# Optimization experiments

Measured on AMD Instinct MI355X. Metric: run time of the kernel, lower is better.

The kernel has to match this reference:

```python
import jax, jax.numpy as jnp
import numpy as np

B, F, N = 64, 32, 36
REGION, HIDDEN, ATT = 1024, 1024, 1024
FEAT2 = REGION + 2 * HIDDEN  # temp_attn feat_size = 3072


def setup_inputs() -> dict:
    key = jax.random.key(0)
    ks = jax.random.split(key, 12)
    s = 0.02
    return {
        "frame_feats": jax.random.normal(ks[0], (B, F, 2 * HIDDEN), jnp.float32),
        "object_feats": jax.random.normal(ks[1], (B, F, N, REGION), jnp.float32),
        "hidden_state": jax.random.normal(ks[2], (B, HIDDEN), jnp.float32),
        # spatial attention params (torch Linear: y = x @ W.T + b)
        "s_wh_w": jax.random.normal(ks[3], (ATT, HIDDEN), jnp.float32) * s,
        "s_wh_b": jnp.zeros((ATT,), jnp.float32),
        "s_wv_w": jax.random.normal(ks[4], (ATT, REGION), jnp.float32) * s,
        "s_wv_b": jnp.zeros((ATT,), jnp.float32),
        "s_wa_w": jax.random.normal(ks[5], (ATT,), jnp.float32) * s,
        # temporal attention params (att_size = hidden_size here)
        "t_wh_w": jax.random.normal(ks[6], (HIDDEN, HIDDEN), jnp.float32) * s,
        "t_wh_b": jnp.zeros((HIDDEN,), jnp.float32),
        "t_wv_w": jax.random.normal(ks[7], (HIDDEN, FEAT2), jnp.float32) * s,
        "t_wv_b": jnp.zeros((HIDDEN,), jnp.float32),
        "t_wa_w": jax.random.normal(ks[8], (HIDDEN,), jnp.float32) * s,
    }


def reference(frame_feats, object_feats, hidden_state,
              s_wh_w, s_wh_b, s_wv_w, s_wv_b, s_wa_w,
              t_wh_w, t_wh_b, t_wv_w, t_wv_b, t_wa_w):
    # ---- spatial attention over num_boxes, per (batch, frame) ----
    # v: [B,F,N,ATT]; key proj broadcasts over frames and boxes
    v = jnp.einsum('bfnd,ad->bfna', object_feats, s_wv_w) + s_wv_b
    h = hidden_state @ s_wh_w.T + s_wh_b            # [B,ATT]
    score = jnp.tanh(v + h[:, None, None, :]) @ s_wa_w  # [B,F,N]
    alpha = jax.nn.softmax(score, axis=-1)
    obj_att = jnp.einsum('bfn,bfnd->bfd', alpha, object_feats)  # [B,F,REGION]

    # ---- temporal attention over frames ----
    feat = jnp.concatenate([obj_att, frame_feats], axis=-1)     # [B,F,FEAT2]
    v2 = jnp.einsum('bfd,ad->bfa', feat, t_wv_w) + t_wv_b       # [B,F,HIDDEN]
    h2 = hidden_state @ t_wh_w.T + t_wh_b                       # [B,HIDDEN]
    score2 = jnp.tanh(v2 + h2[:, None, :]) @ t_wa_w             # [B,F]
    beta = jax.nn.softmax(score2, axis=-1)
    loc_feat = jnp.einsum('bf,bfd->bd', beta, feat)             # [B,FEAT2]
    return loc_feat
```

## Files before the change

### kernel.cpp

```cpp
#include <hip/hip_runtime.h>
#include <hip/hip_bf16.h>
#include <stdint.h>

#define BATCH  64
#define NFRAME 32
#define NBOX   36
#define REGION 1024
#define HIDDEN 1024
#define ATTSZ  1024
#define FEAT2  3072
#define M_S (BATCH * NFRAME * NBOX)
#define M_T (BATCH * NFRAME)

typedef __attribute__((ext_vector_type(8))) short bf16x8;
typedef __attribute__((ext_vector_type(4))) float f32x4;

__device__ __forceinline__ unsigned short f2bf(float f) {
  union { float f; uint32_t u; } v; v.f = f;
  return (unsigned short)((v.u + 0x7FFFu + ((v.u >> 16) & 1u)) >> 16);
}
__device__ __forceinline__ float bf2f(unsigned short u) {
  union { uint32_t u; float f; } v; v.u = (uint32_t)u << 16; return v.f;
}
__device__ __forceinline__ float fast_tanh(float x) {
  float e = __expf(2.f * x);
  return 1.f - 2.f / (e + 1.f);
}
__device__ __forceinline__ void gload_lds16(const unsigned short* g, unsigned short* l) {
  __builtin_amdgcn_global_load_lds(
      (const __attribute__((address_space(1))) unsigned int*)g,
      (__attribute__((address_space(3))) unsigned int*)l, 16, 0, 0);
}

__global__ __launch_bounds__(256) void cast_f32_bf16(
    const float* __restrict__ in, unsigned short* __restrict__ out, long n) {
  long i = ((long)blockIdx.x * 256 + threadIdx.x) * 8;
  if (i >= n) return;
  float4 a = *(const float4*)(in + i);
  float4 b = *(const float4*)(in + i + 4);
  ushort4 lo; lo.x = f2bf(a.x); lo.y = f2bf(a.y); lo.z = f2bf(a.z); lo.w = f2bf(a.w);
  ushort4 hi; hi.x = f2bf(b.x); hi.y = f2bf(b.y); hi.z = f2bf(b.z); hi.w = f2bf(b.w);
  *(ushort4*)(out + i) = lo;
  *(ushort4*)(out + i + 4) = hi;
}

template<int TM, int TN>
__global__ __launch_bounds__(256, 2) void gemm_tanh_score(
    const unsigned short* __restrict__ A, const unsigned short* __restrict__ W,
    const float* __restrict__ hvec, const float* __restrict__ wa,
    float* __restrict__ score, int K, int rows_per_b)
{
  constexpr int BM = 2 * TM * 16;
  constexpr int BN = 2 * TN * 16;
  __shared__ __align__(16) unsigned short ldsA[BM * 64];
  __shared__ __align__(16) unsigned short ldsW[BN * 64];
  __shared__ float h_tile[BN];
  __shared__ float score_sh[2][BM];

  const int tid  = threadIdx.x;
  const int lane = tid & 63;
  const int wid  = tid >> 6;
  const int wr   = (wid >> 1) * (TM * 16);
  const int wc   = (wid & 1) * (TN * 16);
  const int l15  = lane & 15;
  const int q    = lane >> 4;
  const long r0  = (long)blockIdx.y * BM;
  const int  c0  = blockIdx.x * BN;
  const int srow = lane >> 3;
  const int sgr  = lane & 7;
  const int b0   = (int)(r0 / rows_per_b);

  for (int i = tid; i < BN; i += 256)
    h_tile[i] = hvec[(long)b0 * ATTSZ + c0 + i];
  float wac[TN];
  #pragma unroll
  for (int j = 0; j < TN; ++j) wac[j] = wa[c0 + wc + j * 16 + l15];

  f32x4 acc[TM][TN] = {};

  for (int k0 = 0; k0 < K; k0 += 64) {
    __syncthreads();
    #pragma unroll
    for (int it = 0; it < BM / 32; ++it) {
      int c = wid * (BM / 32) + it;
      gload_lds16(A + (r0 + c * 8 + srow) * (long)K + k0 + sgr * 8, ldsA + c * 512);
    }
    #pragma unroll
    for (int it = 0; it < BN / 32; ++it) {
      int c = wid * (BN / 32) + it;
      gload_lds16(W + ((long)(c0 + c * 8 + srow)) * K + k0 + sgr * 8, ldsW + c * 512);
    }
    __syncthreads();
    #pragma unroll
    for (int s = 0; s < 2; ++s) {
      bf16x8 af[TM], wf[TN];
      #pragma unroll
      for (int i = 0; i < TM; ++i)
        af[i] = *(const bf16x8*)(ldsA + (wr + i * 16 + l15) * 64 + s * 32 + q * 8);
      #pragma unroll
      for (int j = 0; j < TN; ++j)
        wf[j] = *(const bf16x8*)(ldsW + (wc + j * 16 + l15) * 64 + s * 32 + q * 8);
      #pragma unroll
      for (int i = 0; i < TM; ++i)
        #pragma unroll
        for (int j = 0; j < TN; ++j)
          acc[i][j] = __builtin_amdgcn_mfma_f32_16x16x32_bf16(af[i], wf[j], acc[i][j], 0, 0, 0);
    }
  }

  #pragma unroll
  for (int i = 0; i < TM; ++i) {
    #pragma unroll
    for (int r = 0; r < 4; ++r) {
      float part = 0.f;
      #pragma unroll
      for (int j = 0; j < TN; ++j) {
        float x = acc[i][j][r] + h_tile[wc + j * 16 + l15];
        part += fast_tanh(x) * wac[j];
      }
      part += __shfl_xor(part, 1); part += __shfl_xor(part, 2);
      part += __shfl_xor(part, 4); part += __shfl_xor(part, 8);
      if (l15 == 0) score_sh[wid & 1][wr + i * 16 + q * 4 + r] = part;
    }
  }
  __syncthreads();
  if (tid < BM)
    atomicAdd(score + r0 + tid, score_sh[0][tid] + score_sh[1][tid]);
}

__global__ __launch_bounds__(256) void hidden_proj(
    const float* __restrict__ hidden,
    const float* __restrict__ s_wh_w, const float* __restrict__ s_wh_b,
    const float* __restrict__ s_wv_b,
    const float* __restrict__ t_wh_w, const float* __restrict__ t_wh_b,
    const float* __restrict__ t_wv_b,
    float* __restrict__ h_s, float* __restrict__ h_t)
{
  const float *W, *b1, *b2;
  float* out;
  if (blockIdx.y == 0) { W = s_wh_w; b1 = s_wh_b; b2 = s_wv_b; out = h_s; }
  else                 { W = t_wh_w; b1 = t_wh_b; b2 = t_wv_b; out = h_t; }
  const int lane = threadIdx.x & 63;
  const int wid  = threadIdx.x >> 6;
  const int a    = blockIdx.x * 4 + wid;
  __shared__ float hs[64 * 256];
  float acc[64];
  #pragma unroll
  for (int b = 0; b < 64; ++b) acc[b] = 0.f;

  for (int dc = 0; dc < 4; ++dc) {
    __syncthreads();
    for (int i = threadIdx.x; i < 4096; i += 256) {
      int b = i >> 6, d4 = i & 63;
      *(float4*)(hs + b * 256 + d4 * 4) =
          *(const float4*)(hidden + b * 1024 + dc * 256 + d4 * 4);
    }
    __syncthreads();
    float4 w4 = *(const float4*)(W + (long)a * 1024 + dc * 256 + lane * 4);
    #pragma unroll
    for (int b = 0; b < 64; ++b) {
      float4 h4 = *(const float4*)(hs + b * 256 + lane * 4);
      acc[b] += w4.x * h4.x + w4.y * h4.y + w4.z * h4.z + w4.w * h4.w;
    }
  }
  #pragma unroll
  for (int b = 0; b < 64; ++b) {
    #pragma unroll
    for (int off = 1; off < 64; off <<= 1)
      acc[b] += __shfl_xor(acc[b], off);
  }
  float res = 0.f;
  #pragma unroll
  for (int b = 0; b < 64; ++b)
    if (lane == b) res = acc[b];
  out[lane * 1024 + a] = res + b1[a] + b2[a];
}

__global__ __launch_bounds__(256) void spatial_softmax_obj_bf16(
    const unsigned short* __restrict__ objb, const float* __restrict__ score,
    const float* __restrict__ frame, float* __restrict__ feat,
    unsigned short* __restrict__ featb)
{
  const int bf = blockIdx.x;
  __shared__ float alpha[NBOX];
  if (threadIdx.x < 64) {
    int n = threadIdx.x;
    float v = (n < NBOX) ? score[bf * NBOX + n] : -1e30f;
    float m = v;
    #pragma unroll
    for (int off = 32; off; off >>= 1) m = fmaxf(m, __shfl_xor(m, off));
    float e = (n < NBOX) ? __expf(v - m) : 0.f;
    float ssum = e;
    #pragma unroll
    for (int off = 32; off; off >>= 1) ssum += __shfl_xor(ssum, off);
    if (n < NBOX) alpha[n] = e / ssum;
  }
  __syncthreads();
  const unsigned short* base = objb + (long)bf * NBOX * REGION;
  float4 av = {0.f, 0.f, 0.f, 0.f};
  for (int n = 0; n < NBOX; ++n) {
    float al = alpha[n];
    ushort4 o = *(const ushort4*)(base + n * REGION + threadIdx.x * 4);
    av.x += al * bf2f(o.x); av.y += al * bf2f(o.y);
    av.z += al * bf2f(o.z); av.w += al * bf2f(o.w);
  }
  float* frow = feat + (long)bf * FEAT2;
  unsigned short* fbrow = featb + (long)bf * FEAT2;
  *(float4*)(frow + threadIdx.x * 4) = av;
  ushort4 avb; avb.x = f2bf(av.x); avb.y = f2bf(av.y); avb.z = f2bf(av.z); avb.w = f2bf(av.w);
  *(ushort4*)(fbrow + threadIdx.x * 4) = avb;
  const float* fsrc = frame + (long)bf * 2 * HIDDEN;
  #pragma unroll
  for (int c = 0; c < 2; ++c) {
    float4 v = *(const float4*)(fsrc + (threadIdx.x + c * 256) * 4);
    *(float4*)(frow + REGION + (threadIdx.x + c * 256) * 4) = v;
    ushort4 vb; vb.x = f2bf(v.x); vb.y = f2bf(v.y); vb.z = f2bf(v.z); vb.w = f2bf(v.w);
    *(ushort4*)(fbrow + REGION + (threadIdx.x + c * 256) * 4) = vb;
  }
}

__global__ __launch_bounds__(256) void temporal_out(
    const float* __restrict__ score2, const float* __restrict__ feat,
    float* __restrict__ out)
{
  const int b = blockIdx.x;
  __shared__ float beta[NFRAME];
  if (threadIdx.x < 64) {
    int f = threadIdx.x;
    float v = (f < NFRAME) ? score2[b * NFRAME + f] : -1e30f;
    float m = v;
    #pragma unroll
    for (int off = 32; off; off >>= 1) m = fmaxf(m, __shfl_xor(m, off));
    float e = (f < NFRAME) ? __expf(v - m) : 0.f;
    float ssum = e;
    #pragma unroll
    for (int off = 32; off; off >>= 1) ssum += __shfl_xor(ssum, off);
    if (f < NFRAME) beta[f] = e / ssum;
  }
  __syncthreads();
  #pragma unroll
  for (int c = 0; c < 3; ++c) {
    int col = (threadIdx.x + c * 256) * 4;
    float4 av = {0.f, 0.f, 0.f, 0.f};
    for (int f = 0; f < NFRAME; ++f) {
      float bw = beta[f];
      float4 v = *(const float4*)(feat + (long)(b * NFRAME + f) * FEAT2 + col);
      av.x += bw * v.x; av.y += bw * v.y; av.z += bw * v.z; av.w += bw * v.w;
    }
    *(float4*)(out + (long)b * FEAT2 + col) = av;
  }
}

#define FBM 128
#define FBN 128
#define FBK 64
#define LDKP 72
__global__ __launch_bounds__(256) void fused_gemm_tanh_score_f32(
    const float* __restrict__ A, const float* __restrict__ W,
    const float* __restrict__ hvec, const float* __restrict__ wa,
    float* __restrict__ score, int M, int K, int rows_per_b)
{
  __shared__ unsigned short ldsA[FBM * LDKP];
  __shared__ unsigned short ldsW[FBN * LDKP];
  const int tid  = threadIdx.x;
  const int lane = tid & 63;
  const int wid  = tid >> 6;
  const int wr   = (wid >> 1) * 64;
  const int wc   = (wid & 1) * 64;
  const int l15  = lane & 15;
  const int q    = lane >> 4;
  const long r0  = (long)blockIdx.y * FBM;
  const int  c0  = blockIdx.x * FBN;

  f32x4 acc[4][4] = {};
  for (int k0 = 0; k0 < K; k0 += FBK) {
    __syncthreads();
    #pragma unroll
    for (int it = 0; it < 8; ++it) {
      int c = tid + it * 256;
      int row = c >> 4, qb = c & 15;
      float4 s = *(const float4*)(A + (r0 + row) * (long)K + k0 + qb * 4);
      ushort4 d; d.x = f2bf(s.x); d.y = f2bf(s.y); d.z = f2bf(s.z); d.w = f2bf(s.w);
      *(ushort4*)(ldsA + row * LDKP + qb * 4) = d;
    }
    #pragma unroll
    for (int it = 0; it < 8; ++it) {
      int c = tid + it * 256;
      int row = c >> 4, qb = c & 15;
      float4 s = *(const float4*)(W + (c0 + row) * (long)K + k0 + qb * 4);
      ushort4 d; d.x = f2bf(s.x); d.y = f2bf(s.y); d.z = f2bf(s.z); d.w = f2bf(s.w);
      *(ushort4*)(ldsW + row * LDKP + qb * 4) = d;
    }
    __syncthreads();
    #pragma unroll
    for (int s = 0; s < 2; ++s) {
      bf16x8 af[4], bfr[4];
      #pragma unroll
      for (int i = 0; i < 4; ++i)
        af[i] = *(const bf16x8*)(ldsA + (wr + i * 16 + l15) * LDKP + s * 32 + q * 8);
      #pragma unroll
      for (int j = 0; j < 4; ++j)
        bfr[j] = *(const bf16x8*)(ldsW + (wc + j * 16 + l15) * LDKP + s * 32 + q * 8);
      #pragma unroll
      for (int i = 0; i < 4; ++i)
        #pragma unroll
        for (int j = 0; j < 4; ++j)
          acc[i][j] = __builtin_amdgcn_mfma_f32_16x16x32_bf16(af[i], bfr[j], acc[i][j], 0, 0, 0);
    }
  }
  float wac[4];
  #pragma unroll
  for (int j = 0; j < 4; ++j) wac[j] = wa[c0 + wc + j * 16 + l15];
  #pragma unroll
  for (int i = 0; i < 4; ++i) {
    #pragma unroll
    for (int r = 0; r < 4; ++r) {
      int row = (int)r0 + wr + i * 16 + q * 4 + r;
      const float* hrow = hvec + (long)(row / rows_per_b) * ATTSZ;
      float part = 0.f;
      #pragma unroll
      for (int j = 0; j < 4; ++j) {
        float x = acc[i][j][r] + hrow[c0 + wc + j * 16 + l15];
        part += fast_tanh(x) * wac[j];
      }
      part += __shfl_xor(part, 1); part += __shfl_xor(part, 2);
      part += __shfl_xor(part, 4); part += __shfl_xor(part, 8);
      if (l15 == 0) atomicAdd(score + row, part);
    }
  }
}

__global__ __launch_bounds__(256) void spatial_softmax_obj_f32(
    const float* __restrict__ obj, const float* __restrict__ score,
    const float* __restrict__ frame, float* __restrict__ feat)
{
  const int bf = blockIdx.x;
  __shared__ float alpha[NBOX];
  if (threadIdx.x < 64) {
    int n = threadIdx.x;
    float v = (n < NBOX) ? score[bf * NBOX + n] : -1e30f;
    float m = v;
    #pragma unroll
    for (int off = 32; off; off >>= 1) m = fmaxf(m, __shfl_xor(m, off));
    float e = (n < NBOX) ? __expf(v - m) : 0.f;
    float ssum = e;
    #pragma unroll
    for (int off = 32; off; off >>= 1) ssum += __shfl_xor(ssum, off);
    if (n < NBOX) alpha[n] = e / ssum;
  }
  __syncthreads();
  const float* base = obj + (long)bf * NBOX * REGION;
  float4 av = {0.f, 0.f, 0.f, 0.f};
  for (int n = 0; n < NBOX; ++n) {
    float al = alpha[n];
    float4 o = *(const float4*)(base + n * REGION + threadIdx.x * 4);
    av.x += al * o.x; av.y += al * o.y; av.z += al * o.z; av.w += al * o.w;
  }
  float* frow = feat + (long)bf * FEAT2;
  *(float4*)(frow + threadIdx.x * 4) = av;
  const float4* fsrc = (const float4*)(frame + (long)bf * 2 * HIDDEN);
  float4* fdst = (float4*)(frow + REGION);
  fdst[threadIdx.x]       = fsrc[threadIdx.x];
  fdst[threadIdx.x + 256] = fsrc[threadIdx.x + 256];
}

extern "C" void kernel_launch(void* const* d_in, const int* in_sizes, int n_in,
                              void* d_out, int out_size, void* d_ws, size_t ws_size,
                              hipStream_t stream) {
  const float* frame  = (const float*)d_in[0];
  const float* obj    = (const float*)d_in[1];
  const float* hidden = (const float*)d_in[2];
  const float* s_wh_w = (const float*)d_in[3];
  const float* s_wh_b = (const float*)d_in[4];
  const float* s_wv_w = (const float*)d_in[5];
  const float* s_wv_b = (const float*)d_in[6];
  const float* s_wa_w = (const float*)d_in[7];
  const float* t_wh_w = (const float*)d_in[8];
  const float* t_wh_b = (const float*)d_in[9];
  const float* t_wv_w = (const float*)d_in[10];
  const float* t_wv_b = (const float*)d_in[11];
  const float* t_wa_w = (const float*)d_in[12];
  float* out = (float*)d_out;

  char* p = (char*)d_ws;
  auto alloc = [&](size_t bytes) { char* r = p; p += (bytes + 255) & ~255ull; return r; };
  float* h_s     = (float*)alloc(65536 * 4);
  float* h_t     = (float*)alloc(65536 * 4);
  float* score_s = (float*)alloc((size_t)M_S * 4);
  float* score2  = (float*)alloc((size_t)M_T * 4);
  float* feat    = (float*)alloc((size_t)M_T * FEAT2 * 4);
  unsigned short* objb  = (unsigned short*)alloc((size_t)M_S * REGION * 2);
  unsigned short* featb = (unsigned short*)alloc((size_t)M_T * FEAT2 * 2);
  unsigned short* wvsb  = (unsigned short*)alloc((size_t)ATTSZ * REGION * 2);
  unsigned short* wvtb  = (unsigned short*)alloc((size_t)HIDDEN * FEAT2 * 2);
  size_t needed = (size_t)(p - (char*)d_ws);
  bool fast = needed <= ws_size;

  hipMemsetAsync(score_s, 0, (size_t)(M_S + M_T) * sizeof(float), stream);
  hidden_proj<<<dim3(256, 2), 256, 0, stream>>>(
      hidden, s_wh_w, s_wh_b, s_wv_b, t_wh_w, t_wh_b, t_wv_b, h_s, h_t);

  if (fast) {
    cast_f32_bf16<<<(M_S * (long)REGION) / 2048, 256, 0, stream>>>(obj, objb, (long)M_S * REGION);
    cast_f32_bf16<<<(ATTSZ * (long)REGION) / 2048, 256, 0, stream>>>(s_wv_w, wvsb, (long)ATTSZ * REGION);
    cast_f32_bf16<<<(HIDDEN * (long)FEAT2) / 2048, 256, 0, stream>>>(t_wv_w, wvtb, (long)HIDDEN * FEAT2);

    gemm_tanh_score<4, 8><<<dim3(4, M_S / 128), 256, 0, stream>>>(
        objb, wvsb, h_s, s_wa_w, score_s, REGION, NFRAME * NBOX);

    spatial_softmax_obj_bf16<<<M_T, 256, 0, stream>>>(objb, score_s, frame, feat, featb);

    gemm_tanh_score<1, 4><<<dim3(8, M_T / 32), 256, 0, stream>>>(
        featb, wvtb, h_t, t_wa_w, score2, FEAT2, NFRAME);
  } else {
    fused_gemm_tanh_score_f32<<<dim3(8, M_S / FBM), 256, 0, stream>>>(
        obj, s_wv_w, h_s, s_wa_w, score_s, M_S, REGION, NFRAME * NBOX);
    spatial_softmax_obj_f32<<<M_T, 256, 0, stream>>>(obj, score_s, frame, feat);
    fused_gemm_tanh_score_f32<<<dim3(8, M_T / FBM), 256, 0, stream>>>(
        feat, t_wv_w, h_t, t_wa_w, score2, M_T, FEAT2, NFRAME);
  }

  temporal_out<<<BATCH, 256, 0, stream>>>(score2, feat, out);
}
```

Measured before the change: 789.5 us.

## Swizzle LDS tiles in bf16 GEMM and remap spatial grid for cache locality

Applies an XOR swizzle to the 16-byte chunk index of each row, both when global_load_lds writes the A and W tiles into LDS and when the MFMA fragments are read back. This is meant to remove LDS bank conflicts on the fragment reads. The spatial GEMM also moves to a 1D grid whose block index is remapped so that groups of 8 row tiles sweep all 4 column tiles together, improving L2 reuse of the object tiles. Small unroll pragmas are added to the softmax-weighted reduction loops.

```diff
diff --git a/kernel.cpp b/kernel.cpp
--- a/kernel.cpp
+++ b/kernel.cpp
@@ -44,7 +44,7 @@
   *(ushort4*)(out + i + 4) = hi;
 }
 
-template<int TM, int TN>
+template<int TM, int TN, bool LINGRID, int NCOLT>
 __global__ __launch_bounds__(256, 2) void gemm_tanh_score(
     const unsigned short* __restrict__ A, const unsigned short* __restrict__ W,
     const float* __restrict__ hvec, const float* __restrict__ wa,
@@ -64,11 +64,20 @@
   const int wc   = (wid & 1) * (TN * 16);
   const int l15  = lane & 15;
   const int q    = lane >> 4;
-  const long r0  = (long)blockIdx.y * BM;
-  const int  c0  = blockIdx.x * BN;
+  const int rl   = l15 & 7;
   const int srow = lane >> 3;
-  const int sgr  = lane & 7;
-  const int b0   = (int)(r0 / rows_per_b);
+  const int sgr  = (lane & 7) ^ srow;
+
+  long r0; int c0;
+  if (LINGRID) {
+    int bid = blockIdx.x;
+    int rt = (bid & 7) + (bid >> (3 + (NCOLT == 4 ? 2 : 3))) * 8;
+    int ct = (bid >> 3) & (NCOLT - 1);
+    r0 = (long)rt * BM; c0 = ct * BN;
+  } else {
+    r0 = (long)blockIdx.y * BM; c0 = blockIdx.x * BN;
+  }
+  const int b0 = (int)(r0 / rows_per_b);
 
   for (int i = tid; i < BN; i += 256)
     h_tile[i] = hvec[(long)b0 * ATTSZ + c0 + i];
@@ -83,23 +92,24 @@
     #pragma unroll
     for (int it = 0; it < BM / 32; ++it) {
       int c = wid * (BM / 32) + it;
-      gload_lds16(A + (r0 + c * 8 + srow) * (long)K + k0 + sgr * 8, ldsA + c * 512);
+      gload_lds16(A + (r0 + c * 8 + srow) * (long)K + k0 + (sgr << 3), ldsA + c * 512);
     }
     #pragma unroll
     for (int it = 0; it < BN / 32; ++it) {
       int c = wid * (BN / 32) + it;
-      gload_lds16(W + ((long)(c0 + c * 8 + srow)) * K + k0 + sgr * 8, ldsW + c * 512);
+      gload_lds16(W + ((long)(c0 + c * 8 + srow)) * K + k0 + (sgr << 3), ldsW + c * 512);
     }
     __syncthreads();
     #pragma unroll
     for (int s = 0; s < 2; ++s) {
       bf16x8 af[TM], wf[TN];
+      const int gsw = ((s * 4 + q) ^ rl) << 3;
       #pragma unroll
       for (int i = 0; i < TM; ++i)
-        af[i] = *(const bf16x8*)(ldsA + (wr + i * 16 + l15) * 64 + s * 32 + q * 8);
+        af[i] = *(const bf16x8*)(ldsA + (wr + i * 16 + l15) * 64 + gsw);
       #pragma unroll
       for (int j = 0; j < TN; ++j)
-        wf[j] = *(const bf16x8*)(ldsW + (wc + j * 16 + l15) * 64 + s * 32 + q * 8);
+        wf[j] = *(const bf16x8*)(ldsW + (wc + j * 16 + l15) * 64 + gsw);
       #pragma unroll
       for (int i = 0; i < TM; ++i)
         #pragma unroll
@@ -198,6 +208,7 @@
   __syncthreads();
   const unsigned short* base = objb + (long)bf * NBOX * REGION;
   float4 av = {0.f, 0.f, 0.f, 0.f};
+  #pragma unroll 4
   for (int n = 0; n < NBOX; ++n) {
     float al = alpha[n];
     ushort4 o = *(const ushort4*)(base + n * REGION + threadIdx.x * 4);
@@ -242,6 +253,7 @@
   for (int c = 0; c < 3; ++c) {
     int col = (threadIdx.x + c * 256) * 4;
     float4 av = {0.f, 0.f, 0.f, 0.f};
+    #pragma unroll 4
     for (int f = 0; f < NFRAME; ++f) {
       float bw = beta[f];
       float4 v = *(const float4*)(feat + (long)(b * NFRAME + f) * FEAT2 + col);
@@ -405,12 +417,12 @@
     cast_f32_bf16<<<(ATTSZ * (long)REGION) / 2048, 256, 0, stream>>>(s_wv_w, wvsb, (long)ATTSZ * REGION);
     cast_f32_bf16<<<(HIDDEN * (long)FEAT2) / 2048, 256, 0, stream>>>(t_wv_w, wvtb, (long)HIDDEN * FEAT2);
 
-    gemm_tanh_score<4, 8><<<dim3(4, M_S / 128), 256, 0, stream>>>(
+    gemm_tanh_score<4, 8, true, 4><<<dim3(4 * (M_S / 128)), 256, 0, stream>>>(
         objb, wvsb, h_s, s_wa_w, score_s, REGION, NFRAME * NBOX);
 
     spatial_softmax_obj_bf16<<<M_T, 256, 0, stream>>>(objb, score_s, frame, feat, featb);
 
-    gemm_tanh_score<1, 4><<<dim3(8, M_T / 32), 256, 0, stream>>>(
+    gemm_tanh_score<1, 4, false, 8><<<dim3(8, M_T / 32), 256, 0, stream>>>(
         featb, wvtb, h_t, t_wa_w, score2, FEAT2, NFRAME);
   } else {
     fused_gemm_tanh_score_f32<<<dim3(8, M_S / FBM), 256, 0, stream>>>(
```

After: 748.8 us. 1.05x faster.
